# Optimization experiments

Measured on AMD Instinct MI355X. Metric: run time of the kernel, lower is better.

## Reference

```python
import jax, jax.numpy as jnp
import numpy as np

B, C, T = 4, 512, 4096


def setup_inputs() -> dict:
    key = jax.random.key(0)
    ks = jax.random.split(key, 9)
    s = 1.0 / np.sqrt(C)
    return {
        "x": jax.random.normal(ks[0], (B, C, T), jnp.float32),
        "Wq": jax.random.normal(ks[1], (C, C), jnp.float32) * s,
        "bq": jax.random.normal(ks[2], (C,), jnp.float32) * 0.01,
        "Wk": jax.random.normal(ks[3], (C, C), jnp.float32) * s,
        "bk": jax.random.normal(ks[4], (C,), jnp.float32) * 0.01,
        "Wv": jax.random.normal(ks[5], (C, C), jnp.float32) * s,
        "bv": jax.random.normal(ks[6], (C,), jnp.float32) * 0.01,
        "Wp": jax.random.normal(ks[7], (C, C), jnp.float32) * s,
        "bp": jax.random.normal(ks[8], (C,), jnp.float32) * 0.01,
    }


def reference(x, Wq, bq, Wk, bk, Wv, bv, Wp, bp):
    # x: [B, C, T]; kernel-size-1 causal convs == pointwise linears over channels.
    b, c, t = x.shape
    q = jnp.einsum('oc,bct->bto', Wq, x) + bq  # [B, T, C]
    k = jnp.einsum('oc,bct->bto', Wk, x) + bk
    v = jnp.einsum('oc,bct->bto', Wv, x) + bv
    scale = jnp.asarray(c, x.dtype) ** -0.5
    w = jnp.einsum('btc,bsc->bts', q, k) * scale  # [B, T, T]
    mask = jnp.tril(jnp.ones((t, t), bool))        # causal: query t attends s<=t
    w = jnp.where(mask, w, -jnp.inf)
    w = jax.nn.softmax(w, axis=-1)
    h = jnp.einsum('bts,bsc->btc', w, v)           # [B, T, C]
    out = jnp.einsum('oc,btc->bot', Wp, h) + bp[None, :, None]  # [B, C, T]
    return x + out
```

## Files before the change

### kernel.cpp

```cpp
#include <hip/hip_runtime.h>

#define NB 4
#define NC 512
#define NT 4096
#define NTILE 528

typedef __attribute__((ext_vector_type(4))) float f32x4;
typedef __attribute__((ext_vector_type(8))) short short8;

typedef const __attribute__((address_space(1))) unsigned int* gp1_t;
typedef __attribute__((address_space(3))) unsigned int* lp3_t;

__device__ __forceinline__ void gload16(const short* g, short* l) {
  __builtin_amdgcn_global_load_lds((gp1_t)g, (lp3_t)l, 16, 0, 0);
}

#define BARRIER()  asm volatile("s_barrier" ::: "memory")
#define WAITVM0()  asm volatile("s_waitcnt vmcnt(0)" ::: "memory")
#define WAITVM4()  asm volatile("s_waitcnt vmcnt(4)" ::: "memory")
#define WAITVM8()  asm volatile("s_waitcnt vmcnt(8)" ::: "memory")
#define WAITVM12() asm volatile("s_waitcnt vmcnt(12)" ::: "memory")

__device__ __forceinline__ short f2bf(float f) {
  union { float f; unsigned u; } v; v.f = f;
  unsigned r = v.u + 0x7fffu + ((v.u >> 16) & 1u);
  return (short)(r >> 16);
}
__device__ __forceinline__ float bf2f(short s) {
  union { unsigned u; float f; } v; v.u = ((unsigned)(unsigned short)s) << 16;
  return v.f;
}

#define SCOL_SWZ(lane) ((((lane) & 3) ^ (((lane) >> 3) & 3)) * 8)
#define FKO_SWZ(lane)  (((((lane) >> 4) ^ (((lane) >> 1) & 3)) & 3) * 8)

template <int NBUF>
__device__ __forceinline__ void gemm_tile(const short* __restrict__ A, int lda,
                                          const short* __restrict__ Bg, int ldb,
                                          int m0, int n0, int ksteps,
                                          f32x4 (&acc)[4][4], short* lds) {
  const int tid  = threadIdx.x;
  const int lane = tid & 63;
  const int wv   = tid >> 6;
  const int wm = (wv >> 1) * 64;
  const int wn = (wv & 1) * 64;
  const int srow = wv * 16 + (lane >> 2);
  const int scol = SCOL_SWZ(lane);
  const int fm  = lane & 15;
  const int fko = FKO_SWZ(lane);

  const short* Ap0 = A  + (size_t)(m0 + srow) * lda + scol;
  const short* Ap1 = Ap0 + (size_t)64 * lda;
  const short* Bp0 = Bg + (size_t)(n0 + srow) * ldb + scol;
  const short* Bp1 = Bp0 + (size_t)64 * ldb;

  auto issue = [&](int kt) {
    short* base = lds + (kt % NBUF) * 8192;
    const int k0 = kt * 32;
    gload16(Ap0 + k0, base + wv * 512);
    gload16(Ap1 + k0, base + 2048 + wv * 512);
    gload16(Bp0 + k0, base + 4096 + wv * 512);
    gload16(Bp1 + k0, base + 6144 + wv * 512);
  };

  issue(0);
#pragma unroll
  for (int p = 1; p < NBUF - 1; ++p)
    if (p < ksteps) issue(p);

  for (int kt = 0; kt < ksteps; ++kt) {
    const short* As = lds + (kt % NBUF) * 8192;
    const short* Bs = As + 4096;
    if constexpr (NBUF == 5) {
      if (kt + 3 < ksteps)      { WAITVM12(); }
      else if (kt + 2 < ksteps) { WAITVM8(); }
      else if (kt + 1 < ksteps) { WAITVM4(); }
      else                      { WAITVM0(); }
    } else {
      if (kt + 1 < ksteps)      { WAITVM4(); }
      else                      { WAITVM0(); }
    }
    BARRIER();
    if constexpr (NBUF == 5) {
      if (kt + 4 < ksteps) issue(kt + 4);
    } else {
      if (kt + 2 < ksteps) issue(kt + 2);
    }
    short8 af[4], bfr[4];
#pragma unroll
    for (int i = 0; i < 4; ++i)
      af[i] = *(const short8*)(As + (wm + i * 16 + fm) * 32 + fko);
#pragma unroll
    for (int j = 0; j < 4; ++j)
      bfr[j] = *(const short8*)(Bs + (wn + j * 16 + fm) * 32 + fko);
#pragma unroll
    for (int i = 0; i < 4; ++i)
#pragma unroll
      for (int j = 0; j < 4; ++j)
        acc[i][j] = __builtin_amdgcn_mfma_f32_16x16x32_bf16(af[i], bfr[j], acc[i][j], 0, 0, 0);
  }
}

#define ACC_INIT                                  \
  f32x4 acc[4][4];                                \
  {                                               \
    const f32x4 z = {0.f, 0.f, 0.f, 0.f};         \
    for (int i = 0; i < 4; ++i)                   \
      for (int j = 0; j < 4; ++j) acc[i][j] = z;  \
  }

#define EPI_IDX                                   \
  const int lane = threadIdx.x & 63;              \
  const int wave = threadIdx.x >> 6;              \
  const int wm = (wave >> 1) * 64;                \
  const int wn = (wave & 1) * 64;

#define GEMM_LDS3 __shared__ short lds[24576];
#define GEMM_LDS5 __shared__ short lds[40960];

__device__ __forceinline__ void xcd_rowchunk(int x, int nrows, int& row, int& chunk) {
  const int xcd  = x & 7;
  const int slot = x >> 3;
  row   = nrows - 1 - (xcd + 8 * (slot >> 2));
  chunk = slot & 3;
}

__device__ __forceinline__ void pv_rowchunk(int x, int z, int& bm, int& chunk) {
  const int xcd  = x & 7;
  const int slot = x >> 3;
  int ridx = slot >> 2;
  if (z >= 2) ridx = 3 - ridx;
  bm = (ridx == 0) ? (31 - xcd)
     : (ridx == 1) ? (23 - xcd)
     : (ridx == 2) ? (8 + xcd)
                   : xcd;
  chunk = slot & 3;
}

__global__ __launch_bounds__(256) void k_transpose(const float* __restrict__ x,
                                                   short* __restrict__ xT) {
  __shared__ float tile[32][33];
  const int b  = blockIdx.z;
  const int t0 = blockIdx.x * 32;
  const int c0 = blockIdx.y * 32;
  const int tx = threadIdx.x & 31;
  const int ty = threadIdx.x >> 5;
  const float* xp = x + ((size_t)b * NC + c0) * NT + t0;
#pragma unroll
  for (int i = 0; i < 32; i += 8)
    tile[ty + i][tx] = xp[(size_t)(ty + i) * NT + tx];
  __syncthreads();
  short* op = xT + ((size_t)b * NT + t0) * NC + c0;
#pragma unroll
  for (int i = 0; i < 32; i += 8)
    op[(size_t)(ty + i) * NC + tx] = f2bf(tile[tx][ty + i]);
}

__global__ __launch_bounds__(256) void k_wcvt(const float* __restrict__ s0, const float* __restrict__ s1,
                                              const float* __restrict__ s2, const float* __restrict__ s3,
                                              short* __restrict__ d0, short* __restrict__ d1,
                                              short* __restrict__ d2, short* __restrict__ d3) {
  const float* s; short* d;
  switch (blockIdx.y) {
    case 0: s = s0; d = d0; break;
    case 1: s = s1; d = d1; break;
    case 2: s = s2; d = d2; break;
    default: s = s3; d = d3; break;
  }
  const int i = (blockIdx.x * 256 + threadIdx.x) * 4;
  const float4 v = *(const float4*)(s + i);
  short4 o;
  o.x = f2bf(v.x); o.y = f2bf(v.y); o.z = f2bf(v.z); o.w = f2bf(v.w);
  *(short4*)(d + i) = o;
}

__global__ __launch_bounds__(256, 3) void k_qkv(const short* __restrict__ xT,
                                                const short* __restrict__ Wq,
                                                const float* __restrict__ bq,
                                                const short* __restrict__ Wk,
                                                const float* __restrict__ bk,
                                                const short* __restrict__ Wv,
                                                const float* __restrict__ bv,
                                                short* __restrict__ Q,
                                                short* __restrict__ K,
                                                short* __restrict__ VT) {
  GEMM_LDS3;
  const int b = blockIdx.z;
  const int y = blockIdx.y;
  int row, chunk;
  xcd_rowchunk((int)blockIdx.x, NT / 128, row, chunk);
  const short* Xb = xT + (size_t)b * NT * NC;
  ACC_INIT;
  if (y < 2) {
    const short* W = (y == 0) ? Wq : Wk;
    const float* bias = (y == 0) ? bq : bk;
    short* O = ((y == 0) ? Q : K) + (size_t)b * NT * NC;
    const int m0 = row * 128;
    const int n0 = chunk * 128;
    gemm_tile<3>(Xb, NC, W, NC, m0, n0, NC / 32, acc, lds);
    EPI_IDX;
#pragma unroll
    for (int j = 0; j < 4; ++j) {
      const int n = n0 + wn + j * 16 + (lane & 15);
      const float bv_ = bias[n];
#pragma unroll
      for (int i = 0; i < 4; ++i) {
        const int mb = m0 + wm + i * 16 + ((lane >> 4) * 4);
#pragma unroll
        for (int r = 0; r < 4; ++r)
          O[(size_t)(mb + r) * NC + n] = f2bf(acc[i][j][r] + bv_);
      }
    }
  } else {
    const int n0 = row * 128;
    const int m0 = chunk * 128;
    gemm_tile<3>(Wv, NC, Xb, NC, m0, n0, NC / 32, acc, lds);
    EPI_IDX;
    short* O = VT + (size_t)b * NC * NT;
#pragma unroll
    for (int j = 0; j < 4; ++j) {
      const int n = n0 + wn + j * 16 + (lane & 15);
#pragma unroll
      for (int i = 0; i < 4; ++i) {
        const int mb = m0 + wm + i * 16 + ((lane >> 4) * 4);
#pragma unroll
        for (int r = 0; r < 4; ++r)
          O[(size_t)(mb + r) * NT + n] = f2bf(acc[i][j][r] + bv[mb + r]);
      }
    }
  }
}

__global__ __launch_bounds__(256, 3) void k_scores(const short* __restrict__ Q,
                                                   const short* __restrict__ K,
                                                   short* __restrict__ P,
                                                   float* __restrict__ Lrow) {
  const int p = (((int)blockIdx.x & 7) * 66) + ((int)blockIdx.x >> 3);
  int bm = 0, bn = 0;
  {
    int base = 0;
    for (int sr = 0; sr < 4; ++sr) {
      bool done = false;
      for (int sc = 0; sc <= sr; ++sc) {
        const int sz = (sc == sr) ? 36 : 64;
        if (p < base + sz) {
          const int q = p - base;
          int i, j;
          if (sc == sr) {
            i = 0;
            while ((i + 1) * (i + 2) / 2 <= q) ++i;
            j = q - i * (i + 1) / 2;
          } else { i = q >> 3; j = q & 7; }
          bm = sr * 8 + i; bn = sc * 8 + j;
          done = true; break;
        }
        base += sz;
      }
      if (done) break;
    }
  }
  GEMM_LDS3;
  const int b  = blockIdx.z;
  const int m0 = bm * 128;
  const int n0 = bn * 128;
  ACC_INIT;
  gemm_tile<3>(Q + (size_t)b * NT * NC, NC, K + (size_t)b * NT * NC, NC,
               m0, n0, NC / 32, acc, lds);
  EPI_IDX;
  const float kls = 0.06376070265f;
  const int idx = bm * (bm + 1) / 2 + bn;
  short* Tp = P + ((size_t)b * NTILE + (size_t)idx) * 16384;
  float* Lp = Lrow + (size_t)b * NT;
  float psum[4][4];
#pragma unroll
  for (int i = 0; i < 4; ++i)
#pragma unroll
    for (int r = 0; r < 4; ++r) psum[i][r] = 0.f;

  if (bn < bm) {
#pragma unroll
    for (int j = 0; j < 4; ++j) {
      const int ln = wn + j * 16 + (lane & 15);
#pragma unroll
      for (int i = 0; i < 4; ++i) {
        const int lmb = wm + i * 16 + ((lane >> 4) * 4);
        const float e0 = exp2f(acc[i][j][0] * kls);
        const float e1 = exp2f(acc[i][j][1] * kls);
        const float e2 = exp2f(acc[i][j][2] * kls);
        const float e3 = exp2f(acc[i][j][3] * kls);
        unsigned pk01, pk23;
        asm("v_cvt_pk_bf16_f32 %0, %1, %2" : "=v"(pk01) : "v"(e0), "v"(e1));
        asm("v_cvt_pk_bf16_f32 %0, %1, %2" : "=v"(pk23) : "v"(e2), "v"(e3));
        Tp[(lmb + 0) * 128 + ln] = (short)(pk01 & 0xffffu);
        Tp[(lmb + 1) * 128 + ln] = (short)(pk01 >> 16);
        Tp[(lmb + 2) * 128 + ln] = (short)(pk23 & 0xffffu);
        Tp[(lmb + 3) * 128 + ln] = (short)(pk23 >> 16);
        union { unsigned u; float f; } c0, c1, c2, c3;
        c0.u = pk01 << 16; c1.u = pk01 & 0xffff0000u;
        c2.u = pk23 << 16; c3.u = pk23 & 0xffff0000u;
        psum[i][0] += c0.f; psum[i][1] += c1.f;
        psum[i][2] += c2.f; psum[i][3] += c3.f;
      }
    }
  } else {
#pragma unroll
    for (int j = 0; j < 4; ++j) {
      const int ln = wn + j * 16 + (lane & 15);
      const int n  = n0 + ln;
#pragma unroll
      for (int i = 0; i < 4; ++i) {
        const int lmb = wm + i * 16 + ((lane >> 4) * 4);
#pragma unroll
        for (int r = 0; r < 4; ++r) {
          const int m = m0 + lmb + r;
          float pr = 0.f;
          short pb = 0;
          if (n <= m) {
            pb = f2bf(exp2f(acc[i][j][r] * kls));
            pr = bf2f(pb);
          }
          Tp[(lmb + r) * 128 + ln] = pb;
          psum[i][r] += pr;
        }
      }
    }
  }
#pragma unroll
  for (int i = 0; i < 4; ++i)
#pragma unroll
    for (int r = 0; r < 4; ++r) {
      float v = psum[i][r];
      v += __shfl_xor(v, 1);
      v += __shfl_xor(v, 2);
      v += __shfl_xor(v, 4);
      v += __shfl_xor(v, 8);
      if ((lane & 15) == 0) {
        const int m = m0 + wm + i * 16 + ((lane >> 4) * 4) + r;
        atomicAdd(&Lp[m], v);
      }
    }
}

__global__ __launch_bounds__(256, 2) void k_pv(const short* __restrict__ P,
                                               const short* __restrict__ VT,
                                               const float* __restrict__ Lr,
                                               short* __restrict__ H) {
  GEMM_LDS5;
  const int b = blockIdx.z;
  int bm, chunk;
  pv_rowchunk((int)blockIdx.x, b, bm, chunk);
  const int m0 = bm * 128;
  const int n0 = chunk * 128;
  const int ksteps = (bm + 1) * 4;

  const short* Ptri = P + ((size_t)b * NTILE + (size_t)bm * (bm + 1) / 2) * 16384;
  const short* Bg   = VT + (size_t)b * NC * NT;

  ACC_INIT;
  const int tid  = threadIdx.x;
  const int lane = tid & 63;
  const int wv   = tid >> 6;
  const int wm = (wv >> 1) * 64;
  const int wn = (wv & 1) * 64;
  const int srow = wv * 16 + (lane >> 2);
  const int scol = SCOL_SWZ(lane);
  const int fm  = lane & 15;
  const int fko = FKO_SWZ(lane);

  const short* Bp0 = Bg + (size_t)(n0 + srow) * NT + scol;
  const short* Bp1 = Bp0 + (size_t)64 * NT;

  auto issue = [&](int kt) {
    short* base = lds + (kt % 5) * 8192;
    const short* At = Ptri + (size_t)(kt >> 2) * 16384 + (kt & 3) * 32;
    const short* Ap0 = At + srow * 128 + scol;
    const int k0 = kt * 32;
    gload16(Ap0, base + wv * 512);
    gload16(Ap0 + 64 * 128, base + 2048 + wv * 512);
    gload16(Bp0 + k0, base + 4096 + wv * 512);
    gload16(Bp1 + k0, base + 6144 + wv * 512);
  };

  issue(0);
#pragma unroll
  for (int p = 1; p < 4; ++p)
    if (p < ksteps) issue(p);
  for (int kt = 0; kt < ksteps; ++kt) {
    const short* As = lds + (kt % 5) * 8192;
    const short* Bs = As + 4096;
    if (kt + 3 < ksteps)      { WAITVM12(); }
    else if (kt + 2 < ksteps) { WAITVM8(); }
    else if (kt + 1 < ksteps) { WAITVM4(); }
    else                      { WAITVM0(); }
    BARRIER();
    if (kt + 4 < ksteps) issue(kt + 4);
    short8 af[4], bfr[4];
#pragma unroll
    for (int i = 0; i < 4; ++i)
      af[i] = *(const short8*)(As + (wm + i * 16 + fm) * 32 + fko);
#pragma unroll
    for (int j = 0; j < 4; ++j)
      bfr[j] = *(const short8*)(Bs + (wn + j * 16 + fm) * 32 + fko);
#pragma unroll
    for (int i = 0; i < 4; ++i)
#pragma unroll
      for (int j = 0; j < 4; ++j)
        acc[i][j] = __builtin_amdgcn_mfma_f32_16x16x32_bf16(af[i], bfr[j], acc[i][j], 0, 0, 0);
  }

  const float* L = Lr + (size_t)b * NT;
  short* Hp = H + (size_t)b * NT * NC;
#pragma unroll
  for (int i = 0; i < 4; ++i) {
    const int mb = m0 + wm + i * 16 + ((lane >> 4) * 4);
    float rinv[4];
#pragma unroll
    for (int r = 0; r < 4; ++r) rinv[r] = 1.f / L[mb + r];
#pragma unroll
    for (int j = 0; j < 4; ++j) {
      const int n = n0 + wn + j * 16 + (lane & 15);
#pragma unroll
      for (int r = 0; r < 4; ++r)
        Hp[(size_t)(mb + r) * NC + n] = f2bf(acc[i][j][r] * rinv[r]);
    }
  }
}

__global__ __launch_bounds__(256, 2) void k_out(const short* __restrict__ W,
                                                const short* __restrict__ H,
                                                const float* __restrict__ bias,
                                                const float* __restrict__ x,
                                                float* __restrict__ out) {
  GEMM_LDS5;
  const int b = blockIdx.z;
  int row, chunk;
  xcd_rowchunk((int)blockIdx.x, NT / 128, row, chunk);
  const int n0 = row * 128;
  const int m0 = chunk * 128;
  ACC_INIT;
  gemm_tile<5>(W, NC, H + (size_t)b * NT * NC, NC, m0, n0, NC / 32, acc, lds);
  EPI_IDX;
#pragma unroll
  for (int j = 0; j < 4; ++j) {
    const int n = n0 + wn + j * 16 + (lane & 15);
#pragma unroll
    for (int i = 0; i < 4; ++i) {
      const int mb = m0 + wm + i * 16 + ((lane >> 4) * 4);
#pragma unroll
      for (int r = 0; r < 4; ++r) {
        const int m = mb + r;
        const size_t idx = ((size_t)b * NC + m) * NT + n;
        out[idx] = acc[i][j][r] + bias[m] + x[idx];
      }
    }
  }
}

extern "C" void kernel_launch(void* const* d_in, const int* in_sizes, int n_in,
                              void* d_out, int out_size, void* d_ws, size_t ws_size,
                              hipStream_t stream) {
  (void)in_sizes; (void)n_in; (void)out_size; (void)ws_size;
  const float* x  = (const float*)d_in[0];
  const float* Wq = (const float*)d_in[1];
  const float* bq = (const float*)d_in[2];
  const float* Wk = (const float*)d_in[3];
  const float* bk = (const float*)d_in[4];
  const float* Wv = (const float*)d_in[5];
  const float* bv = (const float*)d_in[6];
  const float* Wp = (const float*)d_in[7];
  const float* bp = (const float*)d_in[8];
  float* out = (float*)d_out;

  char* ws = (char*)d_ws;
  size_t off = 0;
  auto alloc = [&](size_t bytes) { char* p = ws + off; off += bytes; return p; };
  short* xT  = (short*)alloc((size_t)NB * NT * NC * 2);
  short* Qb  = (short*)alloc((size_t)NB * NT * NC * 2);
  short* Kb  = (short*)alloc((size_t)NB * NT * NC * 2);
  short* VTb = (short*)alloc((size_t)NB * NC * NT * 2);
  short* Hb  = (short*)alloc((size_t)NB * NT * NC * 2);
  short* Wqb = (short*)alloc((size_t)NC * NC * 2);
  short* Wkb = (short*)alloc((size_t)NC * NC * 2);
  short* Wvb = (short*)alloc((size_t)NC * NC * 2);
  short* Wpb = (short*)alloc((size_t)NC * NC * 2);
  float* Lr  = (float*)alloc((size_t)NB * NT * 4);
  short* Pb  = (short*)alloc((size_t)NB * NTILE * 16384 * 2);

  hipMemsetAsync(Lr, 0, (size_t)NB * NT * 4, stream);

  const dim3 blk(256);
  k_wcvt<<<dim3(NC * NC / 1024, 4), blk, 0, stream>>>(Wq, Wk, Wv, Wp, Wqb, Wkb, Wvb, Wpb);

  k_transpose<<<dim3(NT / 32, NC / 32, NB), blk, 0, stream>>>(x, xT);

  k_qkv<<<dim3(128, 3, NB), blk, 0, stream>>>(xT, Wqb, bq, Wkb, bk, Wvb, bv, Qb, Kb, VTb);

  k_scores<<<dim3(NTILE, 1, NB), blk, 0, stream>>>(Qb, Kb, Pb, Lr);
  k_pv<<<dim3(128, 1, NB), blk, 0, stream>>>(Pb, VTb, Lr, Hb);
  k_out<<<dim3(128, 1, NB), blk, 0, stream>>>(Wpb, Hb, bp, x, out);
}
```

Baseline: 273.8 us.

## Make score blocks persistent over three tiles and merge preprocessing kernels

The scores kernel now has each block process three consecutive score tiles. The global-to-LDS pipeline runs continuously across tile boundaries, so loads for the next tile overlap the epilogue of the current one, and the grid shrinks to a third. The transpose and weight-conversion kernels are merged into one launch to drop a kernel boundary. The cost is less parallelism in the scores grid, with only 704 blocks in total, and epilogue work inside the main loop, which may raise register pressure.

```diff
diff --git a/kernel.cpp b/kernel.cpp
--- a/kernel.cpp
+++ b/kernel.cpp
@@ -137,41 +137,65 @@
   chunk = slot & 3;
 }
 
-__global__ __launch_bounds__(256) void k_transpose(const float* __restrict__ x,
-                                                   short* __restrict__ xT) {
-  __shared__ float tile[32][33];
-  const int b  = blockIdx.z;
-  const int t0 = blockIdx.x * 32;
-  const int c0 = blockIdx.y * 32;
-  const int tx = threadIdx.x & 31;
-  const int ty = threadIdx.x >> 5;
-  const float* xp = x + ((size_t)b * NC + c0) * NT + t0;
-#pragma unroll
-  for (int i = 0; i < 32; i += 8)
-    tile[ty + i][tx] = xp[(size_t)(ty + i) * NT + tx];
-  __syncthreads();
-  short* op = xT + ((size_t)b * NT + t0) * NC + c0;
-#pragma unroll
-  for (int i = 0; i < 32; i += 8)
-    op[(size_t)(ty + i) * NC + tx] = f2bf(tile[tx][ty + i]);
-}
-
-__global__ __launch_bounds__(256) void k_wcvt(const float* __restrict__ s0, const float* __restrict__ s1,
-                                              const float* __restrict__ s2, const float* __restrict__ s3,
-                                              short* __restrict__ d0, short* __restrict__ d1,
-                                              short* __restrict__ d2, short* __restrict__ d3) {
-  const float* s; short* d;
-  switch (blockIdx.y) {
-    case 0: s = s0; d = d0; break;
-    case 1: s = s1; d = d1; break;
-    case 2: s = s2; d = d2; break;
-    default: s = s3; d = d3; break;
-  }
-  const int i = (blockIdx.x * 256 + threadIdx.x) * 4;
-  const float4 v = *(const float4*)(s + i);
-  short4 o;
-  o.x = f2bf(v.x); o.y = f2bf(v.y); o.z = f2bf(v.z); o.w = f2bf(v.w);
-  *(short4*)(d + i) = o;
+__device__ __forceinline__ void score_decode(int p, int& bm, int& bn) {
+  int base = 0;
+  for (int sr = 0; sr < 4; ++sr) {
+    for (int sc = 0; sc <= sr; ++sc) {
+      const int sz = (sc == sr) ? 36 : 64;
+      if (p < base + sz) {
+        const int q = p - base;
+        int i, j;
+        if (sc == sr) {
+          i = 0;
+          while ((i + 1) * (i + 2) / 2 <= q) ++i;
+          j = q - i * (i + 1) / 2;
+        } else { i = q >> 3; j = q & 7; }
+        bm = sr * 8 + i; bn = sc * 8 + j;
+        return;
+      }
+      base += sz;
+    }
+  }
+}
+
+__global__ __launch_bounds__(256) void k_pre(const float* __restrict__ x,
+                                             short* __restrict__ xT,
+                                             const float* __restrict__ s0, const float* __restrict__ s1,
+                                             const float* __restrict__ s2, const float* __restrict__ s3,
+                                             short* __restrict__ d0, short* __restrict__ d1,
+                                             short* __restrict__ d2, short* __restrict__ d3) {
+  if (blockIdx.y < 16) {
+    __shared__ float tile[32][33];
+    const int b  = blockIdx.z;
+    const int t0 = blockIdx.x * 32;
+    const int c0 = blockIdx.y * 32;
+    const int tx = threadIdx.x & 31;
+    const int ty = threadIdx.x >> 5;
+    const float* xp = x + ((size_t)b * NC + c0) * NT + t0;
+#pragma unroll
+    for (int i = 0; i < 32; i += 8)
+      tile[ty + i][tx] = xp[(size_t)(ty + i) * NT + tx];
+    __syncthreads();
+    short* op = xT + ((size_t)b * NT + t0) * NC + c0;
+#pragma unroll
+    for (int i = 0; i < 32; i += 8)
+      op[(size_t)(ty + i) * NC + tx] = f2bf(tile[tx][ty + i]);
+  } else {
+    const int mat   = (blockIdx.y - 16) * 2 + (blockIdx.z & 1);
+    const int chunk = blockIdx.x + (blockIdx.z >> 1) * 128;
+    const float* s; short* d;
+    switch (mat) {
+      case 0: s = s0; d = d0; break;
+      case 1: s = s1; d = d1; break;
+      case 2: s = s2; d = d2; break;
+      default: s = s3; d = d3; break;
+    }
+    const int i = (chunk * 256 + threadIdx.x) * 4;
+    const float4 v = *(const float4*)(s + i);
+    short4 o;
+    o.x = f2bf(v.x); o.y = f2bf(v.y); o.z = f2bf(v.z); o.w = f2bf(v.w);
+    *(short4*)(d + i) = o;
+  }
 }
 
 __global__ __launch_bounds__(256, 3) void k_qkv(const short* __restrict__ xT,
@@ -235,110 +259,152 @@
                                                    const short* __restrict__ K,
                                                    short* __restrict__ P,
                                                    float* __restrict__ Lrow) {
-  const int p = (((int)blockIdx.x & 7) * 66) + ((int)blockIdx.x >> 3);
-  int bm = 0, bn = 0;
-  {
-    int base = 0;
-    for (int sr = 0; sr < 4; ++sr) {
-      bool done = false;
-      for (int sc = 0; sc <= sr; ++sc) {
-        const int sz = (sc == sr) ? 36 : 64;
-        if (p < base + sz) {
-          const int q = p - base;
-          int i, j;
-          if (sc == sr) {
-            i = 0;
-            while ((i + 1) * (i + 2) / 2 <= q) ++i;
-            j = q - i * (i + 1) / 2;
-          } else { i = q >> 3; j = q & 7; }
-          bm = sr * 8 + i; bn = sc * 8 + j;
-          done = true; break;
+  GEMM_LDS3;
+  const int b = blockIdx.z;
+  const int x = blockIdx.x;
+  const int p0 = ((x & 7) * 66) + (x >> 3) * 3;
+
+  int bmv[3], bnv[3];
+#pragma unroll
+  for (int t = 0; t < 3; ++t) score_decode(p0 + t, bmv[t], bnv[t]);
+
+  const int tid  = threadIdx.x;
+  const int lane = tid & 63;
+  const int wv   = tid >> 6;
+  const int wm = (wv >> 1) * 64;
+  const int wn = (wv & 1) * 64;
+  const int srow = wv * 16 + (lane >> 2);
+  const int scol = SCOL_SWZ(lane);
+  const int fm  = lane & 15;
+  const int fko = FKO_SWZ(lane);
+
+  const short* Qp = Q + (size_t)b * NT * NC;
+  const short* Kp = K + (size_t)b * NT * NC;
+  const short* ApA = Qp + (size_t)(bmv[0] * 128 + srow) * NC + scol;
+  const short* BpA = Kp + (size_t)(bnv[0] * 128 + srow) * NC + scol;
+  const short* ApB = Qp + (size_t)(bmv[1] * 128 + srow) * NC + scol;
+  const short* BpB = Kp + (size_t)(bnv[1] * 128 + srow) * NC + scol;
+  const short* ApC = Qp + (size_t)(bmv[2] * 128 + srow) * NC + scol;
+  const short* BpC = Kp + (size_t)(bnv[2] * 128 + srow) * NC + scol;
+
+  auto issue = [&](int g) {
+    short* base = lds + (g % 3) * 8192;
+    const int k0 = (g & 15) * 32;
+    const short *a, *bb;
+    if (g < 16)      { a = ApA; bb = BpA; }
+    else if (g < 32) { a = ApB; bb = BpB; }
+    else             { a = ApC; bb = BpC; }
+    gload16(a + k0,                       base + wv * 512);
+    gload16(a + (size_t)64 * NC + k0,     base + 2048 + wv * 512);
+    gload16(bb + k0,                      base + 4096 + wv * 512);
+    gload16(bb + (size_t)64 * NC + k0,    base + 6144 + wv * 512);
+  };
+
+  const float kls = 0.06376070265f;
+  float* Lp = Lrow + (size_t)b * NT;
+
+  ACC_INIT;
+  issue(0); issue(1);
+  for (int gkt = 0; gkt < 48; ++gkt) {
+    const short* As = lds + (gkt % 3) * 8192;
+    const short* Bs = As + 4096;
+    if (gkt + 1 < 48) { WAITVM4(); } else { WAITVM0(); }
+    BARRIER();
+    if (gkt + 2 < 48) issue(gkt + 2);
+    short8 af[4], bfr[4];
+#pragma unroll
+    for (int i = 0; i < 4; ++i)
+      af[i] = *(const short8*)(As + (wm + i * 16 + fm) * 32 + fko);
+#pragma unroll
+    for (int j = 0; j < 4; ++j)
+      bfr[j] = *(const short8*)(Bs + (wn + j * 16 + fm) * 32 + fko);
+#pragma unroll
+    for (int i = 0; i < 4; ++i)
+#pragma unroll
+      for (int j = 0; j < 4; ++j)
+        acc[i][j] = __builtin_amdgcn_mfma_f32_16x16x32_bf16(af[i], bfr[j], acc[i][j], 0, 0, 0);
+
+    if ((gkt & 15) == 15) {
+      const int t  = gkt >> 4;
+      const int bm = (t == 0) ? bmv[0] : (t == 1) ? bmv[1] : bmv[2];
+      const int bn = (t == 0) ? bnv[0] : (t == 1) ? bnv[1] : bnv[2];
+      const int m0 = bm * 128, n0 = bn * 128;
+      short* Tp = P + ((size_t)b * NTILE + (size_t)(bm * (bm + 1) / 2 + bn)) * 16384;
+      float psum[4][4];
+#pragma unroll
+      for (int i = 0; i < 4; ++i)
+#pragma unroll
+        for (int r = 0; r < 4; ++r) psum[i][r] = 0.f;
+
+      if (bn < bm) {
+#pragma unroll
+        for (int j = 0; j < 4; ++j) {
+          const int ln = wn + j * 16 + (lane & 15);
+#pragma unroll
+          for (int i = 0; i < 4; ++i) {
+            const int lmb = wm + i * 16 + ((lane >> 4) * 4);
+            const float e0 = exp2f(acc[i][j][0] * kls);
+            const float e1 = exp2f(acc[i][j][1] * kls);
+            const float e2 = exp2f(acc[i][j][2] * kls);
+            const float e3 = exp2f(acc[i][j][3] * kls);
+            unsigned pk01, pk23;
+            asm("v_cvt_pk_bf16_f32 %0, %1, %2" : "=v"(pk01) : "v"(e0), "v"(e1));
+            asm("v_cvt_pk_bf16_f32 %0, %1, %2" : "=v"(pk23) : "v"(e2), "v"(e3));
+            Tp[(lmb + 0) * 128 + ln] = (short)(pk01 & 0xffffu);
+            Tp[(lmb + 1) * 128 + ln] = (short)(pk01 >> 16);
+            Tp[(lmb + 2) * 128 + ln] = (short)(pk23 & 0xffffu);
+            Tp[(lmb + 3) * 128 + ln] = (short)(pk23 >> 16);
+            union { unsigned u; float f; } c0, c1, c2, c3;
+            c0.u = pk01 << 16; c1.u = pk01 & 0xffff0000u;
+            c2.u = pk23 << 16; c3.u = pk23 & 0xffff0000u;
+            psum[i][0] += c0.f; psum[i][1] += c1.f;
+            psum[i][2] += c2.f; psum[i][3] += c3.f;
+          }
         }
-        base += sz;
-      }
-      if (done) break;
-    }
-  }
-  GEMM_LDS3;
-  const int b  = blockIdx.z;
-  const int m0 = bm * 128;
-  const int n0 = bn * 128;
-  ACC_INIT;
-  gemm_tile<3>(Q + (size_t)b * NT * NC, NC, K + (size_t)b * NT * NC, NC,
-               m0, n0, NC / 32, acc, lds);
-  EPI_IDX;
-  const float kls = 0.06376070265f;
-  const int idx = bm * (bm + 1) / 2 + bn;
-  short* Tp = P + ((size_t)b * NTILE + (size_t)idx) * 16384;
-  float* Lp = Lrow + (size_t)b * NT;
-  float psum[4][4];
-#pragma unroll
-  for (int i = 0; i < 4; ++i)
-#pragma unroll
-    for (int r = 0; r < 4; ++r) psum[i][r] = 0.f;
-
-  if (bn < bm) {
-#pragma unroll
-    for (int j = 0; j < 4; ++j) {
-      const int ln = wn + j * 16 + (lane & 15);
-#pragma unroll
-      for (int i = 0; i < 4; ++i) {
-        const int lmb = wm + i * 16 + ((lane >> 4) * 4);
-        const float e0 = exp2f(acc[i][j][0] * kls);
-        const float e1 = exp2f(acc[i][j][1] * kls);
-        const float e2 = exp2f(acc[i][j][2] * kls);
-        const float e3 = exp2f(acc[i][j][3] * kls);
-        unsigned pk01, pk23;
-        asm("v_cvt_pk_bf16_f32 %0, %1, %2" : "=v"(pk01) : "v"(e0), "v"(e1));
-        asm("v_cvt_pk_bf16_f32 %0, %1, %2" : "=v"(pk23) : "v"(e2), "v"(e3));
-        Tp[(lmb + 0) * 128 + ln] = (short)(pk01 & 0xffffu);
-        Tp[(lmb + 1) * 128 + ln] = (short)(pk01 >> 16);
-        Tp[(lmb + 2) * 128 + ln] = (short)(pk23 & 0xffffu);
-        Tp[(lmb + 3) * 128 + ln] = (short)(pk23 >> 16);
-        union { unsigned u; float f; } c0, c1, c2, c3;
-        c0.u = pk01 << 16; c1.u = pk01 & 0xffff0000u;
-        c2.u = pk23 << 16; c3.u = pk23 & 0xffff0000u;
-        psum[i][0] += c0.f; psum[i][1] += c1.f;
-        psum[i][2] += c2.f; psum[i][3] += c3.f;
-      }
-    }
-  } else {
-#pragma unroll
-    for (int j = 0; j < 4; ++j) {
-      const int ln = wn + j * 16 + (lane & 15);
-      const int n  = n0 + ln;
-#pragma unroll
-      for (int i = 0; i < 4; ++i) {
-        const int lmb = wm + i * 16 + ((lane >> 4) * 4);
-#pragma unroll
-        for (int r = 0; r < 4; ++r) {
-          const int m = m0 + lmb + r;
-          float pr = 0.f;
-          short pb = 0;
-          if (n <= m) {
-            pb = f2bf(exp2f(acc[i][j][r] * kls));
-            pr = bf2f(pb);
+      } else {
+#pragma unroll
+        for (int j = 0; j < 4; ++j) {
+          const int ln = wn + j * 16 + (lane & 15);
+          const int n  = n0 + ln;
+#pragma unroll
+          for (int i = 0; i < 4; ++i) {
+            const int lmb = wm + i * 16 + ((lane >> 4) * 4);
+#pragma unroll
+            for (int r = 0; r < 4; ++r) {
+              const int m = m0 + lmb + r;
+              float pr = 0.f;
+              short pb = 0;
+              if (n <= m) {
+                pb = f2bf(exp2f(acc[i][j][r] * kls));
+                pr = bf2f(pb);
+              }
+              Tp[(lmb + r) * 128 + ln] = pb;
+              psum[i][r] += pr;
+            }
           }
-          Tp[(lmb + r) * 128 + ln] = pb;
-          psum[i][r] += pr;
         }
       }
-    }
-  }
-#pragma unroll
-  for (int i = 0; i < 4; ++i)
-#pragma unroll
-    for (int r = 0; r < 4; ++r) {
-      float v = psum[i][r];
-      v += __shfl_xor(v, 1);
-      v += __shfl_xor(v, 2);
-      v += __shfl_xor(v, 4);
-      v += __shfl_xor(v, 8);
-      if ((lane & 15) == 0) {
-        const int m = m0 + wm + i * 16 + ((lane >> 4) * 4) + r;
-        atomicAdd(&Lp[m], v);
-      }
-    }
+#pragma unroll
+      for (int i = 0; i < 4; ++i)
+#pragma unroll
+        for (int r = 0; r < 4; ++r) {
+          float v = psum[i][r];
+          v += __shfl_xor(v, 1);
+          v += __shfl_xor(v, 2);
+          v += __shfl_xor(v, 4);
+          v += __shfl_xor(v, 8);
+          if ((lane & 15) == 0) {
+            const int m = m0 + wm + i * 16 + ((lane >> 4) * 4) + r;
+            atomicAdd(&Lp[m], v);
+          }
+        }
+      const f32x4 z = {0.f, 0.f, 0.f, 0.f};
+#pragma unroll
+      for (int i = 0; i < 4; ++i)
+#pragma unroll
+        for (int j = 0; j < 4; ++j) acc[i][j] = z;
+    }
+  }
 }
 
 __global__ __launch_bounds__(256, 2) void k_pv(const short* __restrict__ P,
@@ -489,13 +555,12 @@
   hipMemsetAsync(Lr, 0, (size_t)NB * NT * 4, stream);
 
   const dim3 blk(256);
-  k_wcvt<<<dim3(NC * NC / 1024, 4), blk, 0, stream>>>(Wq, Wk, Wv, Wp, Wqb, Wkb, Wvb, Wpb);
-
-  k_transpose<<<dim3(NT / 32, NC / 32, NB), blk, 0, stream>>>(x, xT);
+  k_pre<<<dim3(NT / 32, 18, NB), blk, 0, stream>>>(x, xT, Wq, Wk, Wv, Wp,
+                                                   Wqb, Wkb, Wvb, Wpb);
 
   k_qkv<<<dim3(128, 3, NB), blk, 0, stream>>>(xT, Wqb, bq, Wkb, bk, Wvb, bv, Qb, Kb, VTb);
 
-  k_scores<<<dim3(NTILE, 1, NB), blk, 0, stream>>>(Qb, Kb, Pb, Lr);
+  k_scores<<<dim3(176, 1, NB), blk, 0, stream>>>(Qb, Kb, Pb, Lr);
   k_pv<<<dim3(128, 1, NB), blk, 0, stream>>>(Pb, VTb, Lr, Hb);
   k_out<<<dim3(128, 1, NB), blk, 0, stream>>>(Wpb, Hb, bp, x, out);
 }
```

After: 345.1 us. 26.1% more time.
